# Kernel optimization log

Measured on AMD Instinct MI355X. Metric: run time of the kernel, lower is better.

Reference implementation:

```python
import jax, jax.numpy as jnp
import numpy as np

NEG = -1e10
EPS = 1e-5
H = 4  # num_heads


def layer_norm(y, g, b):
    m = jnp.mean(y, axis=-1, keepdims=True)
    v = jnp.mean((y - m) ** 2, axis=-1, keepdims=True)
    return (y - m) * jax.lax.rsqrt(v + EPS) * g + b


def setup_inputs() -> dict:
    key = jax.random.key(0)
    B, N, C = 16, 1024, 256
    ks = jax.random.split(key, 12)
    std = 0.1  # matches trunc_normal_(std=0.1) init
    inp = {
        "x": jax.random.normal(ks[0], (B, N, C), jnp.float32),
        "K": jax.random.normal(ks[1], (B, N, N), jnp.float32),
        "n1": jax.random.randint(ks[2], (B,), 8, 33),
        "n2": jax.random.randint(ks[3], (B,), 8, 33),
        "qkv_w": jax.random.normal(ks[4], (3 * C, C), jnp.float32) * std,
        "qkv_b": jnp.zeros((3 * C,), jnp.float32),
        "proj_w": jax.random.normal(ks[5], (C, C), jnp.float32) * std,
        "proj_b": jnp.zeros((C,), jnp.float32),
        "ln1_g": jnp.ones((C,), jnp.float32),
        "ln1_b": jnp.zeros((C,), jnp.float32),
        "ln2_g": jnp.ones((C,), jnp.float32),
        "ln2_b": jnp.zeros((C,), jnp.float32),
        "fc1_w": jax.random.normal(ks[6], (4 * C, C), jnp.float32) * std,
        "fc1_b": jnp.zeros((4 * C,), jnp.float32),
        "fc2_w": jax.random.normal(ks[7], (C, 4 * C), jnp.float32) * std,
        "fc2_b": jnp.zeros((C,), jnp.float32),
    }
    return inp


def reference(x, K, n1, n2, qkv_w, qkv_b, proj_w, proj_b,
              ln1_g, ln1_b, ln2_g, ln2_b, fc1_w, fc1_b, fc2_w, fc2_b):
    B, N, C = x.shape
    D = C // H
    scale = D ** -0.5

    # --- attention block ---
    h = layer_norm(x, ln1_g, ln1_b)
    qkv = (h @ qkv_w.T + qkv_b).reshape(B, N, 3, H, D)
    qkv = jnp.transpose(qkv, (2, 0, 3, 1, 4))  # [3,B,H,N,D]
    q, k, v = qkv[0], qkv[1], qkv[2]

    attn = jnp.einsum('bhnd,bhmd->bhnm', q, k) * scale  # [B,H,N,N]

    # per-sample dynamic block mask: rows>=n1*n2 fully masked; cols>=n1*n2 masked
    nrc = (n1 * n2)[:, None]                  # [B,1]
    invalid = jnp.arange(N)[None, :] >= nrc   # [B,N]
    mask = invalid[:, :, None] | invalid[:, None, :]  # [B,N,N]
    attn = jnp.where(mask[:, None], NEG, attn)
    attn = attn + K[:, None]                  # broadcast K over heads

    a = jax.nn.softmax(attn, axis=-1)
    o = jnp.einsum('bhnm,bhmd->bhnd', a, v)
    o = jnp.transpose(o, (0, 2, 1, 3)).reshape(B, N, C)
    x = x + (o @ proj_w.T + proj_b)

    # --- MLP block (exact GELU as torch nn.GELU) ---
    h2 = layer_norm(x, ln2_g, ln2_b)
    m = jax.nn.gelu(h2 @ fc1_w.T + fc1_b, approximate=False)
    m = m @ fc2_w.T + fc2_b
    return x + m
```

## Files before the change

### kernel.cpp

```cpp
#include <hip/hip_runtime.h>
#include <math.h>
#include <stdint.h>

constexpr int Bc = 16, Nn = 1024, Cc = 256, Hh = 4;
constexpr int Mrows = Bc * Nn;
constexpr float EPSV = 1e-5f;

typedef __attribute__((ext_vector_type(4))) float f32x4;
typedef __attribute__((ext_vector_type(8))) short bf16x8;

__device__ inline float wave_reduce_sum(float v) {
#pragma unroll
  for (int m = 32; m >= 1; m >>= 1) v += __shfl_xor(v, m);
  return v;
}

__device__ inline short f2bf(float f) {
  uint32_t u = __builtin_bit_cast(uint32_t, f);
  u = (u + 0x7fffu + ((u >> 16) & 1u)) >> 16;
  return (short)u;
}
__device__ inline float bf2f(short s) {
  uint32_t u = ((uint32_t)(uint16_t)s) << 16;
  return __builtin_bit_cast(float, u);
}

__device__ inline float gelu_fast(float x) {
  float x2 = x * x;
  float u = x * (0.7978845608028654f + 0.0356774081f * x2);
  float e = __builtin_amdgcn_exp2f(u * 2.8853900817779268f);
  return x * (1.f - __builtin_amdgcn_rcpf(e + 1.f));
}

#define GLDS(gptr, lptr)                                             \
  __builtin_amdgcn_global_load_lds(                                  \
      (const __attribute__((address_space(1))) void*)(gptr),         \
      (__attribute__((address_space(3))) void*)(lptr), 16, 0, 0)

__global__ __launch_bounds__(256)
void cvt_all(const float* __restrict__ s0, short* __restrict__ d0,
             const float* __restrict__ s1, short* __restrict__ d1,
             const float* __restrict__ s2, short* __restrict__ d2,
             const float* __restrict__ s3, short* __restrict__ d3) {
  int bid = blockIdx.x;
  const float* s;
  short* d;
  int base;
  if (bid < 192)      { s = s0; d = d0; base = bid; }
  else if (bid < 256) { s = s1; d = d1; base = bid - 192; }
  else if (bid < 512) { s = s2; d = d2; base = bid - 256; }
  else                { s = s3; d = d3; base = bid - 512; }
  int i = (base * 256 + threadIdx.x) * 4;
  float4 v = *(const float4*)(s + i);
  short4 o;
  o.x = f2bf(v.x); o.y = f2bf(v.y); o.z = f2bf(v.z); o.w = f2bf(v.w);
  *(short4*)(d + i) = o;
}

__global__ __launch_bounds__(256)
void ln_kernel(const float* __restrict__ x, const float* __restrict__ g,
               const float* __restrict__ b, short* __restrict__ h) {
  int row = blockIdx.x * 4 + (threadIdx.x >> 6);
  int lane = threadIdx.x & 63;
  const float4* xr = (const float4*)(x + (size_t)row * Cc);
  float4 v = xr[lane];
  float s = v.x + v.y + v.z + v.w;
  float sq = v.x * v.x + v.y * v.y + v.z * v.z + v.w * v.w;
  s = wave_reduce_sum(s);
  sq = wave_reduce_sum(sq);
  float mean = s * (1.f / Cc);
  float var = sq * (1.f / Cc) - mean * mean;
  float inv = rsqrtf(var + EPSV);
  float4 gg = ((const float4*)g)[lane];
  float4 bb = ((const float4*)b)[lane];
  short4 o;
  o.x = f2bf((v.x - mean) * inv * gg.x + bb.x);
  o.y = f2bf((v.y - mean) * inv * gg.y + bb.y);
  o.z = f2bf((v.z - mean) * inv * gg.z + bb.z);
  o.w = f2bf((v.w - mean) * inv * gg.w + bb.w);
  *(short4*)(h + (size_t)row * Cc + lane * 4) = o;
}

__global__ __launch_bounds__(256)
void qkv_mfma(const short* __restrict__ A, const short* __restrict__ Bw,
              const float* __restrict__ bias, short* __restrict__ qkp,
              short* __restrict__ vtp) {
  __shared__ __align__(16) short As[128 * 64];
  __shared__ __align__(16) short Bs[128 * 64];
  int t = threadIdx.x;
  int w = t >> 6, lane = t & 63;
  int wm = w >> 1, wn = w & 1;
  int l16 = lane & 15, lhi = lane >> 4;
  int m0 = blockIdx.y * 128, n0 = blockIdx.x * 128;
  const bool vblk = (n0 >= 512);
  f32x4 acc[4][4] = {};

  for (int k0 = 0; k0 < 256; k0 += 64) {
    __syncthreads();
#pragma unroll
    for (int i = 0; i < 4; ++i) {
      int cc = i * 256 + t;
      int r = cc >> 3, sl = cc & 7, ssl = sl ^ (r & 7);
      GLDS(A + (size_t)(m0 + r) * 256 + k0 + ssl * 8, &As[cc * 8]);
      GLDS(Bw + (size_t)(n0 + r) * 256 + k0 + ssl * 8, &Bs[cc * 8]);
    }
    asm volatile("s_waitcnt vmcnt(0)" ::: "memory");
    __syncthreads();
    if (!vblk) {
#pragma unroll
      for (int ks = 0; ks < 2; ++ks) {
        bf16x8 af[4], bg[4];
#pragma unroll
        for (int mi = 0; mi < 4; ++mi) {
          int row = wm * 64 + mi * 16 + l16;
          af[mi] = *(const bf16x8*)&As[row * 64 + ((ks * 32 + lhi * 8) ^ ((row & 7) << 3))];
        }
#pragma unroll
        for (int ni = 0; ni < 4; ++ni) {
          int row = wn * 64 + ni * 16 + l16;
          bg[ni] = *(const bf16x8*)&Bs[row * 64 + ((ks * 32 + lhi * 8) ^ ((row & 7) << 3))];
        }
#pragma unroll
        for (int mi = 0; mi < 4; ++mi)
#pragma unroll
          for (int ni = 0; ni < 4; ++ni)
            acc[mi][ni] = __builtin_amdgcn_mfma_f32_16x16x32_bf16(
                af[mi], bg[ni], acc[mi][ni], 0, 0, 0);
      }
    } else {
#pragma unroll
      for (int ks = 0; ks < 2; ++ks) {
        bf16x8 af[4], bg[4];
#pragma unroll
        for (int mi = 0; mi < 4; ++mi) {
          int row = wm * 64 + mi * 16 + l16;
          af[mi] = *(const bf16x8*)&As[row * 64 + ((ks * 32 + lhi * 8) ^ ((row & 7) << 3))];
        }
#pragma unroll
        for (int ni = 0; ni < 4; ++ni) {
          int row = wn * 64 + ni * 16 + l16;
          bg[ni] = *(const bf16x8*)&Bs[row * 64 + ((ks * 32 + lhi * 8) ^ ((row & 7) << 3))];
        }
#pragma unroll
        for (int mi = 0; mi < 4; ++mi)
#pragma unroll
          for (int ni = 0; ni < 4; ++ni)
            acc[mi][ni] = __builtin_amdgcn_mfma_f32_16x16x32_bf16(
                bg[ni], af[mi], acc[mi][ni], 0, 0, 0);
      }
    }
  }

  if (!vblk) {
    const bool isq = (n0 < 256);
#pragma unroll
    for (int mi = 0; mi < 4; ++mi) {
      int mbase = m0 + wm * 64 + mi * 16 + lhi * 4;
#pragma unroll
      for (int ni = 0; ni < 4; ++ni) {
        int n = n0 + wn * 64 + ni * 16 + l16;
        int s = n >> 8, hh = (n >> 6) & 3, d = n & 63;
        float bv = bias[n];
#pragma unroll
        for (int r = 0; r < 4; ++r) {
          int m = mbase + r;
          int b = m >> 10, rw = m & 1023;
          float v = acc[mi][ni][r] + bv;
          if (isq) v *= 0.125f;
          qkp[(size_t)s * 4194304 + (((size_t)(b * 4 + hh)) * 1024 + rw) * 64 + d] = f2bf(v);
        }
      }
    }
  } else {
#pragma unroll
    for (int mi = 0; mi < 4; ++mi) {
#pragma unroll
      for (int ni = 0; ni < 4; ++ni) {
#pragma unroll
        for (int r = 0; r < 4; ++r) {
          int n = n0 + wn * 64 + ni * 16 + lhi * 4 + r;
          int hh = (n >> 6) & 3, d = n & 63;
          int m = m0 + wm * 64 + mi * 16 + l16;
          int b = m >> 10, rw = m & 1023;
          float v = acc[mi][ni][r] + bias[n];
          vtp[(((size_t)(b * 4 + hh)) * 64 + d) * 1024 + rw] = f2bf(v);
        }
      }
    }
  }
}

__global__ __launch_bounds__(256)
void vmean_kernel(const short* __restrict__ vt, short* __restrict__ vmb) {
  __shared__ float part[64][4];
  int bh = blockIdx.x;
  int d = threadIdx.x >> 2, seg = threadIdx.x & 3;
  const short* p = vt + (size_t)bh * 65536 + (size_t)d * 1024 + seg * 256;
  float s = 0.f;
  for (int i = 0; i < 256; i += 8) {
    bf16x8 v = *(const bf16x8*)(p + i);
#pragma unroll
    for (int j = 0; j < 8; ++j) s += bf2f(v[j]);
  }
  part[d][seg] = s;
  __syncthreads();
  if (threadIdx.x < 64) {
    int dd = threadIdx.x;
    float tot = part[dd][0] + part[dd][1] + part[dd][2] + part[dd][3];
    vmb[bh * 64 + dd] = f2bf(tot * (1.f / 1024.f));
  }
}

__global__ __launch_bounds__(256)
void fattn_mfma(const short* __restrict__ qpk, const short* __restrict__ kpk,
                const short* __restrict__ vt, const float* __restrict__ Kmat,
                const int* __restrict__ n1, const int* __restrict__ n2,
                const short* __restrict__ vmb, short* __restrict__ o,
                float* __restrict__ pO, float* __restrict__ pL,
                int tiles_per_split) {
  int bh = blockIdx.y, b = bh >> 2, hh = bh & 3;
  int qt = blockIdx.x;
  int row0 = qt * 64;
  int sp = blockIdx.z;
  int nc = n1[b] * n2[b];
  int t = threadIdx.x;
  __shared__ short vms[64];
  if (t < 64) vms[t] = vmb[bh * 64 + t];
  __syncthreads();
  if (row0 >= nc) {
    if (sp == 0) {
      for (int idx = t; idx < 4096; idx += 256) {
        int r = idx >> 6, d = idx & 63;
        o[((size_t)(b * 1024 + row0 + r)) * 256 + hh * 64 + d] = vms[d];
      }
    }
    return;
  }
  int ntiles = (nc + 63) >> 6;
  int nsp = (ntiles + tiles_per_split - 1) / tiles_per_split;
  int jt0 = sp * tiles_per_split;
  if (jt0 >= ntiles) return;
  int jstart = jt0 * 64;
  int jend = min(jstart + tiles_per_split * 64, nc);
  const bool final_out = (nsp == 1);

  __shared__ __align__(16) short Ks[2][64 * 64];
  __shared__ __align__(16) short Vs[2][64 * 64];
  __shared__ __align__(16) short Ps[64 * 64];
  int w = t >> 6, lane = t & 63, l16 = lane & 15, lhi = lane >> 4;

  constexpr float LOG2E = 1.4426950408889634f;
  constexpr float MREF = 12.0f;

  const short* qb = qpk + (size_t)bh * 65536 + (size_t)(row0 + w * 16 + l16) * 64;
  bf16x8 qf0 = *(const bf16x8*)(qb + lhi * 8);
  bf16x8 qf1 = *(const bf16x8*)(qb + 32 + lhi * 8);

  f32x4 accO[4] = {};
  float lsum[4] = {};
  const float* Kb = Kmat + (size_t)b * 1048576 + (size_t)(row0 + w * 16) * 1024;

  f32x4 kvp[4];

#pragma unroll
  for (int i = 0; i < 2; ++i) {
    int cc = i * 256 + t;
    int r = cc >> 3, sl = cc & 7, ssl = sl ^ (r & 7);
    GLDS(kpk + (size_t)bh * 65536 + (size_t)(jstart + r) * 64 + ssl * 8, &Ks[0][cc * 8]);
    GLDS(vt + (size_t)bh * 65536 + (size_t)r * 1024 + jstart + ssl * 8, &Vs[0][cc * 8]);
  }
#pragma unroll
  for (int ni = 0; ni < 4; ++ni)
#pragma unroll
    for (int r = 0; r < 4; ++r)
      kvp[ni][r] =
          (Kb[(size_t)(lhi * 4 + r) * 1024 + jstart + ni * 16 + l16] - MREF) * LOG2E;

  int cur = 0;
  for (int j0 = jstart; j0 < jend; j0 += 64, cur ^= 1) {
    asm volatile("s_waitcnt vmcnt(0)" ::: "memory");
    __syncthreads();

    f32x4 kvc[4];
#pragma unroll
    for (int i = 0; i < 4; ++i) kvc[i] = kvp[i];
    int jn = j0 + 64;
    if (jn < jend) {
      int nxt = cur ^ 1;
#pragma unroll
      for (int i = 0; i < 2; ++i) {
        int cc = i * 256 + t;
        int r = cc >> 3, sl = cc & 7, ssl = sl ^ (r & 7);
        GLDS(kpk + (size_t)bh * 65536 + (size_t)(jn + r) * 64 + ssl * 8, &Ks[nxt][cc * 8]);
        GLDS(vt + (size_t)bh * 65536 + (size_t)r * 1024 + jn + ssl * 8, &Vs[nxt][cc * 8]);
      }
#pragma unroll
      for (int ni = 0; ni < 4; ++ni)
#pragma unroll
        for (int r = 0; r < 4; ++r)
          kvp[ni][r] =
              (Kb[(size_t)(lhi * 4 + r) * 1024 + jn + ni * 16 + l16] - MREF) * LOG2E;
    }

    f32x4 accS[4] = {};
#pragma unroll
    for (int ks = 0; ks < 2; ++ks) {
#pragma unroll
      for (int ni = 0; ni < 4; ++ni) {
        int row = ni * 16 + l16;
        bf16x8 kf = *(const bf16x8*)&Ks[cur][row * 64 + (((ks * 4 + lhi) ^ (row & 7)) << 3)];
        accS[ni] = __builtin_amdgcn_mfma_f32_16x16x32_bf16(
            ks ? qf1 : qf0, kf, accS[ni], 0, 0, 0);
      }
    }

#pragma unroll
    for (int ni = 0; ni < 4; ++ni) {
      bool valid = (j0 + ni * 16 + l16) < nc;
#pragma unroll
      for (int r = 0; r < 4; ++r) {
        float e = __builtin_amdgcn_exp2f(fmaf(accS[ni][r], LOG2E, kvc[ni][r]));
        e = valid ? e : 0.f;
        lsum[r] += e;
        int prow = w * 16 + lhi * 4 + r;
        int col = ni * 16 + l16;
        Ps[prow * 64 + ((((col >> 3) ^ (prow & 7)) << 3) | (col & 7))] = f2bf(e);
      }
    }

#pragma unroll
    for (int ks = 0; ks < 2; ++ks) {
      int prow = w * 16 + l16;
      bf16x8 pf = *(const bf16x8*)&Ps[prow * 64 + (((ks * 4 + lhi) ^ (prow & 7)) << 3)];
#pragma unroll
      for (int ni = 0; ni < 4; ++ni) {
        int vrow = ni * 16 + l16;
        bf16x8 vf = *(const bf16x8*)&Vs[cur][vrow * 64 + (((ks * 4 + lhi) ^ (vrow & 7)) << 3)];
        accO[ni] = __builtin_amdgcn_mfma_f32_16x16x32_bf16(pf, vf, accO[ni], 0, 0, 0);
      }
    }
  }

#pragma unroll
  for (int r = 0; r < 4; ++r) {
    lsum[r] += __shfl_xor(lsum[r], 1);
    lsum[r] += __shfl_xor(lsum[r], 2);
    lsum[r] += __shfl_xor(lsum[r], 4);
    lsum[r] += __shfl_xor(lsum[r], 8);
  }

  if (final_out) {
#pragma unroll
    for (int ni = 0; ni < 4; ++ni) {
#pragma unroll
      for (int r = 0; r < 4; ++r) {
        int row = row0 + w * 16 + lhi * 4 + r;
        int d = ni * 16 + l16;
        short ov;
        if (row < nc) ov = f2bf(accO[ni][r] * (1.f / lsum[r]));
        else ov = vms[d];
        o[((size_t)(b * 1024 + row)) * 256 + hh * 64 + d] = ov;
      }
    }
  } else {
    float* po = pO + (((size_t)sp * 64 + bh) * 16 + qt) * 4096;
#pragma unroll
    for (int ni = 0; ni < 4; ++ni)
#pragma unroll
      for (int r = 0; r < 4; ++r)
        po[(w * 16 + lhi * 4 + r) * 64 + ni * 16 + l16] = accO[ni][r];
    if (l16 == 0) {
      float* pl = pL + (((size_t)sp * 64 + bh) * 16 + qt) * 64;
#pragma unroll
      for (int r = 0; r < 4; ++r) pl[w * 16 + lhi * 4 + r] = lsum[r];
    }
    if (sp == 0) {
      for (int idx = t; idx < 4096; idx += 256) {
        int r = idx >> 6, d = idx & 63;
        int row = row0 + r;
        if (row >= nc)
          o[((size_t)(b * 1024 + row)) * 256 + hh * 64 + d] = vms[d];
      }
    }
  }
}

__global__ __launch_bounds__(256)
void fattn_combine(const float* __restrict__ pO, const float* __restrict__ pL,
                   const int* __restrict__ n1, const int* __restrict__ n2,
                   short* __restrict__ o, int tiles_per_split) {
  int bh = blockIdx.y, b = bh >> 2, hh = bh & 3;
  int qt = blockIdx.x;
  int row0 = qt * 64;
  int nc = n1[b] * n2[b];
  if (row0 >= nc) return;
  int ntiles = (nc + 63) >> 6;
  int nsp = (ntiles + tiles_per_split - 1) / tiles_per_split;
  if (nsp < 2) return;

  int t = threadIdx.x;
  int q = t >> 2, ds = (t & 3) * 16;
  int row = row0 + q;
  if (row >= nc) return;

  const size_t spstrideO = (size_t)64 * 16 * 4096;
  const size_t spstrideL = (size_t)64 * 16 * 64;
  const float* baseO = pO + ((size_t)bh * 16 + qt) * 4096 + q * 64 + ds;
  const float* baseL = pL + ((size_t)bh * 16 + qt) * 64 + q;

  f32x4 s[4] = {};
  float L = 0.f;
  for (int sp = 0; sp < nsp; ++sp) {
    const float* p = baseO + sp * spstrideO;
#pragma unroll
    for (int i = 0; i < 4; ++i) s[i] += *(const f32x4*)(p + i * 4);
    L += baseL[sp * spstrideL];
  }
  float rl = 1.f / L;
  short* op = o + ((size_t)(b * 1024 + row)) * 256 + hh * 64 + ds;
#pragma unroll
  for (int i = 0; i < 4; ++i) {
    short4 ov;
    ov.x = f2bf(s[i][0] * rl);
    ov.y = f2bf(s[i][1] * rl);
    ov.z = f2bf(s[i][2] * rl);
    ov.w = f2bf(s[i][3] * rl);
    *(short4*)(op + i * 4) = ov;
  }
}

template <bool GELU, bool RES, bool OUTF, bool OUTB>
__global__ __launch_bounds__(256)
void gemm_mfma(const short* __restrict__ A, const short* __restrict__ Bw,
               const float* __restrict__ bias, const float* __restrict__ resid,
               float* __restrict__ Cf, short* __restrict__ Cb,
               int M, int Nd, int Kd) {
  __shared__ __align__(16) short As[128 * 64];
  __shared__ __align__(16) short Bs[128 * 64];
  int t = threadIdx.x;
  int w = t >> 6, lane = t & 63;
  int wm = w >> 1, wn = w & 1;
  int l16 = lane & 15, lhi = lane >> 4;
  int m0 = blockIdx.y * 128, n0 = blockIdx.x * 128;
  f32x4 acc[4][4] = {};

  for (int k0 = 0; k0 < Kd; k0 += 64) {
    __syncthreads();
#pragma unroll
    for (int i = 0; i < 4; ++i) {
      int cc = i * 256 + t;
      int r = cc >> 3, sl = cc & 7, ssl = sl ^ (r & 7);
      GLDS(A + (size_t)(m0 + r) * Kd + k0 + ssl * 8, &As[cc * 8]);
      GLDS(Bw + (size_t)(n0 + r) * Kd + k0 + ssl * 8, &Bs[cc * 8]);
    }
    asm volatile("s_waitcnt vmcnt(0)" ::: "memory");
    __syncthreads();
#pragma unroll
    for (int ks = 0; ks < 2; ++ks) {
      bf16x8 af[4], bg[4];
#pragma unroll
      for (int mi = 0; mi < 4; ++mi) {
        int row = wm * 64 + mi * 16 + l16;
        af[mi] = *(const bf16x8*)&As[row * 64 + ((ks * 32 + lhi * 8) ^ ((row & 7) << 3))];
      }
#pragma unroll
      for (int ni = 0; ni < 4; ++ni) {
        int row = wn * 64 + ni * 16 + l16;
        bg[ni] = *(const bf16x8*)&Bs[row * 64 + ((ks * 32 + lhi * 8) ^ ((row & 7) << 3))];
      }
#pragma unroll
      for (int mi = 0; mi < 4; ++mi)
#pragma unroll
        for (int ni = 0; ni < 4; ++ni)
          acc[mi][ni] = __builtin_amdgcn_mfma_f32_16x16x32_bf16(
              af[mi], bg[ni], acc[mi][ni], 0, 0, 0);
    }
  }
#pragma unroll
  for (int mi = 0; mi < 4; ++mi) {
    int rbase = m0 + wm * 64 + mi * 16 + lhi * 4;
#pragma unroll
    for (int ni = 0; ni < 4; ++ni) {
      int n = n0 + wn * 64 + ni * 16 + l16;
      float bv = bias[n];
#pragma unroll
      for (int r = 0; r < 4; ++r) {
        int m = rbase + r;
        float v = acc[mi][ni][r] + bv;
        if (GELU) v = gelu_fast(v);
        size_t idx = (size_t)m * Nd + n;
        if (RES) v += resid[idx];
        if (OUTF) Cf[idx] = v;
        if (OUTB) Cb[idx] = f2bf(v);
      }
    }
  }
}

template <bool GELU, bool RES, bool OUTF, bool OUTB>
__global__ __launch_bounds__(256)
void gemm64_mfma(const short* __restrict__ A, const short* __restrict__ Bw,
                 const float* __restrict__ bias, const float* __restrict__ resid,
                 float* __restrict__ Cf, short* __restrict__ Cb,
                 int M, int Nd, int Kd) {
  __shared__ __align__(16) short As[64 * 64];
  __shared__ __align__(16) short Bs[128 * 64];
  int t = threadIdx.x;
  int w = t >> 6, lane = t & 63;
  int l16 = lane & 15, lhi = lane >> 4;
  int m0 = blockIdx.y * 64, n0 = blockIdx.x * 128;
  f32x4 acc[4][2] = {};

  for (int k0 = 0; k0 < Kd; k0 += 64) {
    __syncthreads();
#pragma unroll
    for (int i = 0; i < 2; ++i) {
      int cc = i * 256 + t;
      int r = cc >> 3, sl = cc & 7, ssl = sl ^ (r & 7);
      GLDS(A + (size_t)(m0 + r) * Kd + k0 + ssl * 8, &As[cc * 8]);
    }
#pragma unroll
    for (int i = 0; i < 4; ++i) {
      int cc = i * 256 + t;
      int r = cc >> 3, sl = cc & 7, ssl = sl ^ (r & 7);
      GLDS(Bw + (size_t)(n0 + r) * Kd + k0 + ssl * 8, &Bs[cc * 8]);
    }
    asm volatile("s_waitcnt vmcnt(0)" ::: "memory");
    __syncthreads();
#pragma unroll
    for (int ks = 0; ks < 2; ++ks) {
      bf16x8 af[4], bg[2];
#pragma unroll
      for (int mi = 0; mi < 4; ++mi) {
        int row = mi * 16 + l16;
        af[mi] = *(const bf16x8*)&As[row * 64 + ((ks * 32 + lhi * 8) ^ ((row & 7) << 3))];
      }
#pragma unroll
      for (int ni = 0; ni < 2; ++ni) {
        int row = w * 32 + ni * 16 + l16;
        bg[ni] = *(const bf16x8*)&Bs[row * 64 + ((ks * 32 + lhi * 8) ^ ((row & 7) << 3))];
      }
#pragma unroll
      for (int mi = 0; mi < 4; ++mi)
#pragma unroll
        for (int ni = 0; ni < 2; ++ni)
          acc[mi][ni] = __builtin_amdgcn_mfma_f32_16x16x32_bf16(
              af[mi], bg[ni], acc[mi][ni], 0, 0, 0);
    }
  }
#pragma unroll
  for (int mi = 0; mi < 4; ++mi) {
    int rbase = m0 + mi * 16 + lhi * 4;
#pragma unroll
    for (int ni = 0; ni < 2; ++ni) {
      int n = n0 + w * 32 + ni * 16 + l16;
      float bv = bias[n];
#pragma unroll
      for (int r = 0; r < 4; ++r) {
        int m = rbase + r;
        float v = acc[mi][ni][r] + bv;
        if (GELU) v = gelu_fast(v);
        size_t idx = (size_t)m * Nd + n;
        if (RES) v += resid[idx];
        if (OUTF) Cf[idx] = v;
        if (OUTB) Cb[idx] = f2bf(v);
      }
    }
  }
}

extern "C" void kernel_launch(void* const* d_in, const int* in_sizes, int n_in,
                              void* d_out, int out_size, void* d_ws, size_t ws_size,
                              hipStream_t stream) {
  const float* x      = (const float*)d_in[0];
  const float* Kmat   = (const float*)d_in[1];
  const int*   n1     = (const int*)d_in[2];
  const int*   n2     = (const int*)d_in[3];
  const float* qkv_w  = (const float*)d_in[4];
  const float* qkv_b  = (const float*)d_in[5];
  const float* proj_w = (const float*)d_in[6];
  const float* proj_b = (const float*)d_in[7];
  const float* ln1_g  = (const float*)d_in[8];
  const float* ln1_b  = (const float*)d_in[9];
  const float* ln2_g  = (const float*)d_in[10];
  const float* ln2_b  = (const float*)d_in[11];
  const float* fc1_w  = (const float*)d_in[12];
  const float* fc1_b  = (const float*)d_in[13];
  const float* fc2_w  = (const float*)d_in[14];
  const float* fc2_b  = (const float*)d_in[15];
  float* out = (float*)d_out;

  char* ws = (char*)d_ws;
  constexpr size_t MB = 1024 * 1024;
  short* hb    = (short*)ws;
  short* qkp   = (short*)(ws + 8 * MB);
  short* vtp   = (short*)(ws + 24 * MB);
  short* m1    = (short*)(ws + 8 * MB);
  short* vmb   = (short*)(ws + 40 * MB);
  short* wqkv  = (short*)(ws + 41 * MB);
  short* wproj = (short*)(ws + 42 * MB);
  short* wfc1  = (short*)(ws + 43 * MB);
  short* wfc2  = (short*)(ws + 44 * MB);
  float* pO    = (float*)(ws + 48 * MB);
  float* pL    = (float*)(ws + 116 * MB);
  short* obuf  = hb;
  short* qpk   = qkp;
  short* kpk   = qkp + 4194304;

  const bool split = ws_size >= (size_t)118 * MB;

  cvt_all<<<dim3(768), 256, 0, stream>>>(qkv_w, wqkv, proj_w, wproj,
                                         fc1_w, wfc1, fc2_w, wfc2);
  ln_kernel<<<dim3(Mrows / 4), 256, 0, stream>>>(x, ln1_g, ln1_b, hb);
  qkv_mfma<<<dim3(6, 128), 256, 0, stream>>>(hb, wqkv, qkv_b, qkp, vtp);
  vmean_kernel<<<dim3(Bc * Hh), 256, 0, stream>>>(vtp, vmb);
  if (split) {
    fattn_mfma<<<dim3(Nn / 64, Bc * Hh, 4), 256, 0, stream>>>(
        qpk, kpk, vtp, Kmat, n1, n2, vmb, obuf, pO, pL, 4);
    fattn_combine<<<dim3(Nn / 64, Bc * Hh), 256, 0, stream>>>(
        pO, pL, n1, n2, obuf, 4);
  } else {
    fattn_mfma<<<dim3(Nn / 64, Bc * Hh, 1), 256, 0, stream>>>(
        qpk, kpk, vtp, Kmat, n1, n2, vmb, obuf, pO, pL, 16);
  }
  gemm64_mfma<false, true, true, false><<<dim3(2, 256), 256, 0, stream>>>(
      obuf, wproj, proj_b, x, out, nullptr, Mrows, 256, 256);
  ln_kernel<<<dim3(Mrows / 4), 256, 0, stream>>>(out, ln2_g, ln2_b, hb);
  gemm_mfma<true, false, false, true><<<dim3(8, 128), 256, 0, stream>>>(
      hb, wfc1, fc1_b, nullptr, nullptr, m1, Mrows, 1024, 256);
  gemm64_mfma<false, true, true, false><<<dim3(2, 256), 256, 0, stream>>>(
      m1, wfc2, fc2_b, out, out, nullptr, Mrows, 256, 1024);
}
```

Baseline: 137.2 us.

## Double-buffer LDS tiles in QKV and GEMM kernels to overlap loads with MFMA

Converts the shared-memory A/B tiles in the QKV, 128x128 and 64x128 GEMM kernels into two-stage ping-pong buffers. The next K-slice is issued with global-to-LDS loads before the MFMAs run on the current slice, which is meant to hide global load latency behind compute. This doubles LDS per block (up to 64 KB), which may lower occupancy. Only one barrier now guards each stage, and correctness depends on the wait/sync ordering between the buffers.

```diff
diff --git a/kernel.cpp b/kernel.cpp
--- a/kernel.cpp
+++ b/kernel.cpp
@@ -85,8 +85,8 @@
 void qkv_mfma(const short* __restrict__ A, const short* __restrict__ Bw,
               const float* __restrict__ bias, short* __restrict__ qkp,
               short* __restrict__ vtp) {
-  __shared__ __align__(16) short As[128 * 64];
-  __shared__ __align__(16) short Bs[128 * 64];
+  __shared__ __align__(16) short As[2][128 * 64];
+  __shared__ __align__(16) short Bs[2][128 * 64];
   int t = threadIdx.x;
   int w = t >> 6, lane = t & 63;
   int wm = w >> 1, wn = w & 1;
@@ -95,52 +95,50 @@
   const bool vblk = (n0 >= 512);
   f32x4 acc[4][4] = {};
 
-  for (int k0 = 0; k0 < 256; k0 += 64) {
-    __syncthreads();
-#pragma unroll
-    for (int i = 0; i < 4; ++i) {
-      int cc = i * 256 + t;
-      int r = cc >> 3, sl = cc & 7, ssl = sl ^ (r & 7);
-      GLDS(A + (size_t)(m0 + r) * 256 + k0 + ssl * 8, &As[cc * 8]);
-      GLDS(Bw + (size_t)(n0 + r) * 256 + k0 + ssl * 8, &Bs[cc * 8]);
-    }
+#pragma unroll
+  for (int i = 0; i < 4; ++i) {
+    int cc = i * 256 + t;
+    int r = cc >> 3, sl = cc & 7, ssl = sl ^ (r & 7);
+    GLDS(A + (size_t)(m0 + r) * 256 + ssl * 8, &As[0][cc * 8]);
+    GLDS(Bw + (size_t)(n0 + r) * 256 + ssl * 8, &Bs[0][cc * 8]);
+  }
+
+  int cur = 0;
+  for (int k0 = 0; k0 < 256; k0 += 64, cur ^= 1) {
     asm volatile("s_waitcnt vmcnt(0)" ::: "memory");
     __syncthreads();
-    if (!vblk) {
-#pragma unroll
-      for (int ks = 0; ks < 2; ++ks) {
-        bf16x8 af[4], bg[4];
-#pragma unroll
-        for (int mi = 0; mi < 4; ++mi) {
-          int row = wm * 64 + mi * 16 + l16;
-          af[mi] = *(const bf16x8*)&As[row * 64 + ((ks * 32 + lhi * 8) ^ ((row & 7) << 3))];
-        }
-#pragma unroll
-        for (int ni = 0; ni < 4; ++ni) {
-          int row = wn * 64 + ni * 16 + l16;
-          bg[ni] = *(const bf16x8*)&Bs[row * 64 + ((ks * 32 + lhi * 8) ^ ((row & 7) << 3))];
-        }
+    int kn = k0 + 64;
+    if (kn < 256) {
+      int nxt = cur ^ 1;
+#pragma unroll
+      for (int i = 0; i < 4; ++i) {
+        int cc = i * 256 + t;
+        int r = cc >> 3, sl = cc & 7, ssl = sl ^ (r & 7);
+        GLDS(A + (size_t)(m0 + r) * 256 + kn + ssl * 8, &As[nxt][cc * 8]);
+        GLDS(Bw + (size_t)(n0 + r) * 256 + kn + ssl * 8, &Bs[nxt][cc * 8]);
+      }
+    }
+#pragma unroll
+    for (int ks = 0; ks < 2; ++ks) {
+      bf16x8 af[4], bg[4];
+#pragma unroll
+      for (int mi = 0; mi < 4; ++mi) {
+        int row = wm * 64 + mi * 16 + l16;
+        af[mi] = *(const bf16x8*)&As[cur][row * 64 + ((ks * 32 + lhi * 8) ^ ((row & 7) << 3))];
+      }
+#pragma unroll
+      for (int ni = 0; ni < 4; ++ni) {
+        int row = wn * 64 + ni * 16 + l16;
+        bg[ni] = *(const bf16x8*)&Bs[cur][row * 64 + ((ks * 32 + lhi * 8) ^ ((row & 7) << 3))];
+      }
+      if (!vblk) {
 #pragma unroll
         for (int mi = 0; mi < 4; ++mi)
 #pragma unroll
           for (int ni = 0; ni < 4; ++ni)
             acc[mi][ni] = __builtin_amdgcn_mfma_f32_16x16x32_bf16(
                 af[mi], bg[ni], acc[mi][ni], 0, 0, 0);
-      }
-    } else {
-#pragma unroll
-      for (int ks = 0; ks < 2; ++ks) {
-        bf16x8 af[4], bg[4];
-#pragma unroll
-        for (int mi = 0; mi < 4; ++mi) {
-          int row = wm * 64 + mi * 16 + l16;
-          af[mi] = *(const bf16x8*)&As[row * 64 + ((ks * 32 + lhi * 8) ^ ((row & 7) << 3))];
-        }
-#pragma unroll
-        for (int ni = 0; ni < 4; ++ni) {
-          int row = wn * 64 + ni * 16 + l16;
-          bg[ni] = *(const bf16x8*)&Bs[row * 64 + ((ks * 32 + lhi * 8) ^ ((row & 7) << 3))];
-        }
+      } else {
 #pragma unroll
         for (int mi = 0; mi < 4; ++mi)
 #pragma unroll
@@ -435,8 +433,8 @@
                const float* __restrict__ bias, const float* __restrict__ resid,
                float* __restrict__ Cf, short* __restrict__ Cb,
                int M, int Nd, int Kd) {
-  __shared__ __align__(16) short As[128 * 64];
-  __shared__ __align__(16) short Bs[128 * 64];
+  __shared__ __align__(16) short As[2][128 * 64];
+  __shared__ __align__(16) short Bs[2][128 * 64];
   int t = threadIdx.x;
   int w = t >> 6, lane = t & 63;
   int wm = w >> 1, wn = w & 1;
@@ -444,29 +442,41 @@
   int m0 = blockIdx.y * 128, n0 = blockIdx.x * 128;
   f32x4 acc[4][4] = {};
 
-  for (int k0 = 0; k0 < Kd; k0 += 64) {
-    __syncthreads();
-#pragma unroll
-    for (int i = 0; i < 4; ++i) {
-      int cc = i * 256 + t;
-      int r = cc >> 3, sl = cc & 7, ssl = sl ^ (r & 7);
-      GLDS(A + (size_t)(m0 + r) * Kd + k0 + ssl * 8, &As[cc * 8]);
-      GLDS(Bw + (size_t)(n0 + r) * Kd + k0 + ssl * 8, &Bs[cc * 8]);
-    }
+#pragma unroll
+  for (int i = 0; i < 4; ++i) {
+    int cc = i * 256 + t;
+    int r = cc >> 3, sl = cc & 7, ssl = sl ^ (r & 7);
+    GLDS(A + (size_t)(m0 + r) * Kd + ssl * 8, &As[0][cc * 8]);
+    GLDS(Bw + (size_t)(n0 + r) * Kd + ssl * 8, &Bs[0][cc * 8]);
+  }
+
+  int cur = 0;
+  for (int k0 = 0; k0 < Kd; k0 += 64, cur ^= 1) {
     asm volatile("s_waitcnt vmcnt(0)" ::: "memory");
     __syncthreads();
+    int kn = k0 + 64;
+    if (kn < Kd) {
+      int nxt = cur ^ 1;
+#pragma unroll
+      for (int i = 0; i < 4; ++i) {
+        int cc = i * 256 + t;
+        int r = cc >> 3, sl = cc & 7, ssl = sl ^ (r & 7);
+        GLDS(A + (size_t)(m0 + r) * Kd + kn + ssl * 8, &As[nxt][cc * 8]);
+        GLDS(Bw + (size_t)(n0 + r) * Kd + kn + ssl * 8, &Bs[nxt][cc * 8]);
+      }
+    }
 #pragma unroll
     for (int ks = 0; ks < 2; ++ks) {
       bf16x8 af[4], bg[4];
 #pragma unroll
       for (int mi = 0; mi < 4; ++mi) {
         int row = wm * 64 + mi * 16 + l16;
-        af[mi] = *(const bf16x8*)&As[row * 64 + ((ks * 32 + lhi * 8) ^ ((row & 7) << 3))];
+        af[mi] = *(const bf16x8*)&As[cur][row * 64 + ((ks * 32 + lhi * 8) ^ ((row & 7) << 3))];
       }
 #pragma unroll
       for (int ni = 0; ni < 4; ++ni) {
         int row = wn * 64 + ni * 16 + l16;
-        bg[ni] = *(const bf16x8*)&Bs[row * 64 + ((ks * 32 + lhi * 8) ^ ((row & 7) << 3))];
+        bg[ni] = *(const bf16x8*)&Bs[cur][row * 64 + ((ks * 32 + lhi * 8) ^ ((row & 7) << 3))];
       }
 #pragma unroll
       for (int mi = 0; mi < 4; ++mi)
@@ -503,42 +513,59 @@
                  const float* __restrict__ bias, const float* __restrict__ resid,
                  float* __restrict__ Cf, short* __restrict__ Cb,
                  int M, int Nd, int Kd) {
-  __shared__ __align__(16) short As[64 * 64];
-  __shared__ __align__(16) short Bs[128 * 64];
+  __shared__ __align__(16) short As[2][64 * 64];
+  __shared__ __align__(16) short Bs[2][128 * 64];
   int t = threadIdx.x;
   int w = t >> 6, lane = t & 63;
   int l16 = lane & 15, lhi = lane >> 4;
   int m0 = blockIdx.y * 64, n0 = blockIdx.x * 128;
   f32x4 acc[4][2] = {};
 
-  for (int k0 = 0; k0 < Kd; k0 += 64) {
-    __syncthreads();
-#pragma unroll
-    for (int i = 0; i < 2; ++i) {
-      int cc = i * 256 + t;
-      int r = cc >> 3, sl = cc & 7, ssl = sl ^ (r & 7);
-      GLDS(A + (size_t)(m0 + r) * Kd + k0 + ssl * 8, &As[cc * 8]);
-    }
-#pragma unroll
-    for (int i = 0; i < 4; ++i) {
-      int cc = i * 256 + t;
-      int r = cc >> 3, sl = cc & 7, ssl = sl ^ (r & 7);
-      GLDS(Bw + (size_t)(n0 + r) * Kd + k0 + ssl * 8, &Bs[cc * 8]);
-    }
+#pragma unroll
+  for (int i = 0; i < 2; ++i) {
+    int cc = i * 256 + t;
+    int r = cc >> 3, sl = cc & 7, ssl = sl ^ (r & 7);
+    GLDS(A + (size_t)(m0 + r) * Kd + ssl * 8, &As[0][cc * 8]);
+  }
+#pragma unroll
+  for (int i = 0; i < 4; ++i) {
+    int cc = i * 256 + t;
+    int r = cc >> 3, sl = cc & 7, ssl = sl ^ (r & 7);
+    GLDS(Bw + (size_t)(n0 + r) * Kd + ssl * 8, &Bs[0][cc * 8]);
+  }
+
+  int cur = 0;
+  for (int k0 = 0; k0 < Kd; k0 += 64, cur ^= 1) {
     asm volatile("s_waitcnt vmcnt(0)" ::: "memory");
     __syncthreads();
+    int kn = k0 + 64;
+    if (kn < Kd) {
+      int nxt = cur ^ 1;
+#pragma unroll
+      for (int i = 0; i < 2; ++i) {
+        int cc = i * 256 + t;
+        int r = cc >> 3, sl = cc & 7, ssl = sl ^ (r & 7);
+        GLDS(A + (size_t)(m0 + r) * Kd + kn + ssl * 8, &As[nxt][cc * 8]);
+      }
+#pragma unroll
+      for (int i = 0; i < 4; ++i) {
+        int cc = i * 256 + t;
+        int r = cc >> 3, sl = cc & 7, ssl = sl ^ (r & 7);
+        GLDS(Bw + (size_t)(n0 + r) * Kd + kn + ssl * 8, &Bs[nxt][cc * 8]);
+      }
+    }
 #pragma unroll
     for (int ks = 0; ks < 2; ++ks) {
       bf16x8 af[4], bg[2];
 #pragma unroll
       for (int mi = 0; mi < 4; ++mi) {
         int row = mi * 16 + l16;
-        af[mi] = *(const bf16x8*)&As[row * 64 + ((ks * 32 + lhi * 8) ^ ((row & 7) << 3))];
+        af[mi] = *(const bf16x8*)&As[cur][row * 64 + ((ks * 32 + lhi * 8) ^ ((row & 7) << 3))];
       }
 #pragma unroll
       for (int ni = 0; ni < 2; ++ni) {
         int row = w * 32 + ni * 16 + l16;
-        bg[ni] = *(const bf16x8*)&Bs[row * 64 + ((ks * 32 + lhi * 8) ^ ((row & 7) << 3))];
+        bg[ni] = *(const bf16x8*)&Bs[cur][row * 64 + ((ks * 32 + lhi * 8) ^ ((row & 7) << 3))];
       }
 #pragma unroll
       for (int mi = 0; mi < 4; ++mi)
```

New measurement: 134.1 us. 2.3% less time.
